# Performance work log

Hardware: AMD Instinct MI355X
Metric: run time of the kernel (lower is better)

The kernel has to match this reference:

```python
import jax, jax.numpy as jnp
import numpy as np

EMB = 1024
HEADS = 16
HEAD_DIM = EMB // HEADS
DIM_FF = 4096
EPS = 1e-05


def layer_norm(x, gain, bias):
    # BasicLayerNorm: (x - mean) / (std + eps), std with unbiased=False
    mean = jnp.mean(x, axis=-1, keepdims=True)
    std = jnp.sqrt(jnp.mean((x - mean) ** 2, axis=-1, keepdims=True))
    return gain * ((x - mean) / (std + EPS)) + bias


def setup_inputs() -> dict:
    key = jax.random.key(0)
    ks = jax.random.split(key, 8)
    scale = 1.0 / np.sqrt(EMB)
    x = jax.random.normal(ks[0], (4, 2048, EMB), dtype=jnp.float32)
    Wq = jax.random.normal(ks[1], (EMB, EMB), dtype=jnp.float32) * scale
    Wk = jax.random.normal(ks[2], (EMB, EMB), dtype=jnp.float32) * scale
    Wv = jax.random.normal(ks[3], (EMB, EMB), dtype=jnp.float32) * scale
    Wo = jax.random.normal(ks[4], (EMB, EMB), dtype=jnp.float32) * scale
    W1 = jax.random.normal(ks[5], (EMB, DIM_FF), dtype=jnp.float32) * scale
    b1 = jnp.zeros((DIM_FF,), dtype=jnp.float32)
    W2 = jax.random.normal(ks[6], (DIM_FF, EMB), dtype=jnp.float32) * (1.0 / np.sqrt(DIM_FF))
    b2 = jnp.zeros((EMB,), dtype=jnp.float32)
    gain1 = jnp.ones((EMB,), dtype=jnp.float32)
    bias1 = jnp.zeros((EMB,), dtype=jnp.float32)
    gain2 = jnp.ones((EMB,), dtype=jnp.float32)
    bias2 = jnp.zeros((EMB,), dtype=jnp.float32)
    return dict(x=x, Wq=Wq, Wk=Wk, Wv=Wv, Wo=Wo, W1=W1, b1=b1, W2=W2, b2=b2,
                gain1=gain1, bias1=bias1, gain2=gain2, bias2=bias2)


def reference(x, Wq, Wk, Wv, Wo, W1, b1, W2, b2, gain1, bias1, gain2, bias2):
    b, t, e = x.shape
    h, dk = HEADS, HEAD_DIM
    # QKV projections, split heads -> (b, h, t, dk)
    q = (x @ Wq).reshape(b, t, h, dk).transpose(0, 2, 1, 3)
    k = (x @ Wk).reshape(b, t, h, dk).transpose(0, 2, 1, 3)
    v = (x @ Wv).reshape(b, t, h, dk).transpose(0, 2, 1, 3)
    # scaled dot-product attention
    scores = jnp.einsum('bhqd,bhkd->bhqk', q, k) / jnp.sqrt(jnp.float32(dk))
    attn = jax.nn.softmax(scores, axis=-1)
    ctx = jnp.einsum('bhqk,bhkd->bhqd', attn, v)
    # merge heads and output projection
    merged = ctx.transpose(0, 2, 1, 3).reshape(b, t, e)
    attended = merged @ Wo
    # residual + layer norm 1 (dropout is identity at inference)
    x1 = layer_norm(attended + x, gain1, bias1)
    # feed-forward
    ff = jax.nn.relu(x1 @ W1 + b1) @ W2 + b2
    # residual + layer norm 2
    return layer_norm(ff + x1, gain2, bias2)
```

## Files before the change

kernel.cpp:

```cpp
#include <hip/hip_runtime.h>
#include <hip/hip_bf16.h>
#include <math.h>

#define EMB 1024
#define DIM_FF 4096
#define HEADS 16
#define HD 64
#define TSEQ 2048
#define BATCH 4
#define MROWS (BATCH*TSEQ)
#define LN_EPS 1e-5f

typedef __attribute__((ext_vector_type(8))) short short8;
typedef __attribute__((ext_vector_type(4))) float f32x4;

#define MFMA16(a,b,c) __builtin_amdgcn_mfma_f32_16x16x32_bf16((a),(b),(c),0,0,0)

#define GLOBAL_AS(p) ((const __attribute__((address_space(1))) void*)(p))
#define LDS_AS(p)    ((__attribute__((address_space(3))) void*)(p))

__device__ __forceinline__ unsigned short bf16bits(float f){
    __hip_bfloat16 h = __float2bfloat16(f);
    unsigned short u;
    __builtin_memcpy(&u, &h, 2);
    return u;
}
__device__ __forceinline__ unsigned cvtpk_bf16(float lo, float hi){
    unsigned r;
    asm("v_cvt_pk_bf16_f32 %0, %1, %2" : "=v"(r) : "v"(lo), "v"(hi));
    return r;
}
__device__ __forceinline__ f32x4 ld4bf(const __hip_bfloat16* p){
    ushort4 u = *reinterpret_cast<const ushort4*>(p);
    union{unsigned i; float f;} c0,c1,c2,c3;
    c0.i=(unsigned)u.x<<16; c1.i=(unsigned)u.y<<16; c2.i=(unsigned)u.z<<16; c3.i=(unsigned)u.w<<16;
    f32x4 r; r[0]=c0.f; r[1]=c1.f; r[2]=c2.f; r[3]=c3.f;
    return r;
}

__global__ __launch_bounds__(256)
void cvt_bf16(const float* __restrict__ in, __hip_bfloat16* __restrict__ out, int n4){
    int i = blockIdx.x*256 + threadIdx.x;
    if (i >= n4) return;
    f32x4 v = reinterpret_cast<const f32x4*>(in)[i];
    uint2 o;
    o.x = cvtpk_bf16(v[0], v[1]);
    o.y = cvtpk_bf16(v[2], v[3]);
    *reinterpret_cast<uint2*>(reinterpret_cast<unsigned short*>(out) + (size_t)i*4) = o;
}

__global__ __launch_bounds__(256)
void transpose_cvt4(const float* __restrict__ s0, const float* __restrict__ s1,
                    const float* __restrict__ s2, const float* __restrict__ s3,
                    __hip_bfloat16* __restrict__ out){
    const float* in = blockIdx.z==0 ? s0 : blockIdx.z==1 ? s1 : blockIdx.z==2 ? s2 : s3;
    __hip_bfloat16* dst = out + (size_t)blockIdx.z*1024*1024;
    __shared__ __hip_bfloat16 tile[32][33];
    int bx = blockIdx.x*32, by = blockIdx.y*32;
    int x = bx + threadIdx.x;
    #pragma unroll
    for (int i = threadIdx.y; i < 32; i += 8)
        tile[i][threadIdx.x] = __float2bfloat16(in[(size_t)(by+i)*1024 + x]);
    __syncthreads();
    int xo = by + threadIdx.x;
    #pragma unroll
    for (int i = threadIdx.y; i < 32; i += 8)
        dst[(size_t)(bx+i)*1024 + xo] = tile[threadIdx.x][i];
}

__global__ __launch_bounds__(256)
void transpose_cvt(const float* __restrict__ in, __hip_bfloat16* __restrict__ out, int R, int C){
    __shared__ __hip_bfloat16 tile[32][33];
    int bx = blockIdx.x*32, by = blockIdx.y*32;
    int x = bx + threadIdx.x;
    #pragma unroll
    for (int i = threadIdx.y; i < 32; i += 8)
        tile[i][threadIdx.x] = __float2bfloat16(in[(size_t)(by+i)*C + x]);
    __syncthreads();
    int xo = by + threadIdx.x;
    #pragma unroll
    for (int i = threadIdx.y; i < 32; i += 8)
        out[(size_t)(bx+i)*R + xo] = tile[threadIdx.x][i];
}

template<int EPI>
__global__ __launch_bounds__(256, 2)
void gemm_bt(const __hip_bfloat16* __restrict__ A,
             const __hip_bfloat16* __restrict__ Bt,
             int M, int N, int K,
             __hip_bfloat16* __restrict__ Cb,
             const float* __restrict__ bias)
{
    __shared__ __align__(16) __hip_bfloat16 As[128*32];
    __shared__ __align__(16) __hip_bfloat16 Bs[128*32];
    const int tid = threadIdx.x;
    const int lane = tid & 63;
    const int wid = tid >> 6;
    const int wm = wid >> 1, wn = wid & 1;
    const int row0 = blockIdx.x * 128;
    const int col0 = blockIdx.y * 128;
    const int rA = lane & 15, kg = lane >> 4;

    const int lrow = lane >> 2;
    const int lcol = (lane & 3) << 3;

    f32x4 acc[4][4] = {};

    for (int kt = 0; kt < K; kt += 32) {
        __syncthreads();
        #pragma unroll
        for (int half = 0; half < 2; ++half) {
            const int rbase = (wid << 5) + (half << 4);
            const int r = rbase + lrow;
            __builtin_amdgcn_global_load_lds(
                GLOBAL_AS(A + (size_t)(row0 + r)*K + kt + lcol),
                LDS_AS(&As[rbase*32]), 16, 0, 0);
            __builtin_amdgcn_global_load_lds(
                GLOBAL_AS(Bt + (size_t)(col0 + r)*K + kt + lcol),
                LDS_AS(&Bs[rbase*32]), 16, 0, 0);
        }
        __syncthreads();
        short8 af[4], bfr[4];
        #pragma unroll
        for (int mi = 0; mi < 4; ++mi)
            af[mi] = *reinterpret_cast<const short8*>(&As[(wm*64 + mi*16 + rA)*32 + (kg<<3)]);
        #pragma unroll
        for (int ni = 0; ni < 4; ++ni)
            bfr[ni] = *reinterpret_cast<const short8*>(&Bs[(wn*64 + ni*16 + rA)*32 + (kg<<3)]);
        #pragma unroll
        for (int mi = 0; mi < 4; ++mi)
            #pragma unroll
            for (int ni = 0; ni < 4; ++ni)
                acc[mi][ni] = MFMA16(af[mi], bfr[ni], acc[mi][ni]);
    }

    #pragma unroll
    for (int mi=0; mi<4; ++mi) {
        #pragma unroll
        for (int ni=0; ni<4; ++ni) {
            #pragma unroll
            for (int j=0;j<4;++j){
                float v = acc[mi][ni][j];
                int grow = row0 + wm*64 + mi*16 + (kg<<2) + j;
                int gcol = col0 + wn*64 + ni*16 + rA;
                if constexpr (EPI==3) v += bias[gcol];
                Cb[(size_t)grow*N + gcol] = __float2bfloat16(v);
            }
        }
    }
}

#define GPHASE(P, STAGE_EXPR, WAIT_EXPR) do { \
    short8 af[2][2]; \
    _Pragma("unroll") \
    for (int i_=0;i_<2;++i_){ \
      _Pragma("unroll") \
      for (int kk_=0;kk_<2;++kk_) \
        af[i_][kk_] = *reinterpret_cast<const short8*>(pA + ((2*(P)+i_)*16+rA)*128 + (((kk_<<2)+kg)^swz)*16); \
    } \
    STAGE_EXPR; WAIT_EXPR; \
    __builtin_amdgcn_s_barrier(); \
    __builtin_amdgcn_s_setprio(1); \
    _Pragma("unroll") \
    for (int i_=0;i_<2;++i_){ \
      _Pragma("unroll") \
      for (int ni_=0;ni_<4;++ni_){ \
        acc[2*(P)+i_][ni_] = MFMA16(af[i_][0], bfr[ni_][0], acc[2*(P)+i_][ni_]); \
        acc[2*(P)+i_][ni_] = MFMA16(af[i_][1], bfr[ni_][1], acc[2*(P)+i_][ni_]); \
      } \
    } \
    __builtin_amdgcn_s_setprio(0); \
    __builtin_amdgcn_s_barrier(); \
} while(0)

template<int EPI>
__global__ __launch_bounds__(512, 2)
void gemm256(const __hip_bfloat16* __restrict__ A,
             const __hip_bfloat16* __restrict__ Bt,
             int M, int N, int K,
             __hip_bfloat16* __restrict__ Cb,
             const float* __restrict__ bias,
             __hip_bfloat16* __restrict__ qo,
             __hip_bfloat16* __restrict__ ko,
             __hip_bfloat16* __restrict__ vto)
{
    __shared__ __align__(16) __hip_bfloat16 Al[2][16384];
    __shared__ __align__(16) __hip_bfloat16 Bl[2][16384];
    const int tid = threadIdx.x;
    const int lane = tid & 63;
    const int wid = tid >> 6;
    const int wm = wid >> 2, wn = wid & 3;
    const int row0 = blockIdx.x * 256;
    const int col0 = blockIdx.y * 256;
    const int rA = lane & 15, kg = lane >> 4, swz = rA & 7;
    const int NT = K >> 6;

    const int lr = lane >> 3;
    const int lg = (lane & 7) ^ lr;
    const __hip_bfloat16* sA = A  + (size_t)(row0 + wid*8 + lr)*K + lg*8;
    const __hip_bfloat16* sB = Bt + (size_t)(col0 + wid*8 + lr)*K + lg*8;
    char* dA = (char*)&Al[0][0] + wid*8*128;
    char* dB = (char*)&Bl[0][0] + wid*8*128;

    auto stage = [&](const __hip_bfloat16* s, char* d, int buf, int half, int kt){
        #pragma unroll
        for (int rr = 0; rr < 2; ++rr)
            __builtin_amdgcn_global_load_lds(
                GLOBAL_AS(s + (size_t)(half*128 + rr*64)*K + kt),
                LDS_AS(d + buf*32768 + (half*128 + rr*64)*128), 16, 0, 0);
    };

    f32x4 acc[8][4] = {};

    stage(sA, dA, 0, 0, 0); stage(sA, dA, 0, 1, 0);
    stage(sB, dB, 0, 0, 0); stage(sB, dB, 0, 1, 0);
    stage(sB, dB, 1, 0, 64); stage(sB, dB, 1, 1, 64);
    asm volatile("s_waitcnt vmcnt(4)" ::: "memory");
    __builtin_amdgcn_sched_barrier(0);
    __builtin_amdgcn_s_barrier();

    const char* cA = (const char*)&Al[0][0] + wm*128*128;
    const char* cB = (const char*)&Bl[0][0] + wn*64*128;

    for (int t = 0; t < NT; ++t) {
        const int buf = t & 1;
        const char* pA = cA + buf*32768;
        const char* pB = cB + buf*32768;
        short8 bfr[4][2];
        #pragma unroll
        for (int ni = 0; ni < 4; ++ni)
            #pragma unroll
            for (int kk = 0; kk < 2; ++kk)
                bfr[ni][kk] = *reinterpret_cast<const short8*>(pB + (ni*16+rA)*128 + (((kk<<2)+kg)^swz)*16);

        GPHASE(0, if (t+1 < NT) stage(sA, dA, buf^1, 0, (t+1)*64), );
        GPHASE(1, if (t+1 < NT) stage(sA, dA, buf^1, 1, (t+1)*64), );
        GPHASE(2, if (t+2 < NT) stage(sB, dB, buf,   0, (t+2)*64), );
        GPHASE(3, if (t+2 < NT) stage(sB, dB, buf,   1, (t+2)*64),
            if (t+2 < NT) { asm volatile("s_waitcnt vmcnt(4)" ::: "memory"); }
            else          { asm volatile("s_waitcnt vmcnt(0)" ::: "memory"); }
            __builtin_amdgcn_sched_barrier(0) );
    }

    #pragma unroll
    for (int mi=0; mi<8; ++mi) {
        #pragma unroll
        for (int ni=0; ni<4; ++ni) {
            #pragma unroll
            for (int j=0;j<4;++j){
                float v = acc[mi][ni][j];
                int grow = row0 + wm*128 + mi*16 + (kg<<2) + j;
                int gcol = col0 + wn*64 + ni*16 + rA;
                if constexpr (EPI==0) {
                    int b = grow >> 11, t = grow & 2047;
                    int which = gcol >> 10, hdx = gcol & 1023;
                    int h = hdx >> 6, d = hdx & 63;
                    int bh = b*HEADS + h;
                    if (which==0)      qo[((size_t)bh*TSEQ + t)*HD + d] = __float2bfloat16(v*0.125f);
                    else if (which==1) ko[((size_t)bh*TSEQ + t)*HD + d] = __float2bfloat16(v);
                    else               vto[((size_t)bh*HD + d)*TSEQ + t] = __float2bfloat16(v);
                } else {
                    v += bias[gcol]; v = v > 0.0f ? v : 0.0f;
                    Cb[(size_t)grow*N + gcol] = __float2bfloat16(v);
                }
            }
        }
    }
}

__global__ __launch_bounds__(256, 4)
void attn_fwd(const __hip_bfloat16* __restrict__ q,
              const __hip_bfloat16* __restrict__ k,
              const __hip_bfloat16* __restrict__ vt,
              __hip_bfloat16* __restrict__ merged)
{
    const int wg = (blockIdx.x & 7) * 256 + (blockIdx.x >> 3);
    const int bh = wg >> 5;
    const int qt = wg & 31;
    const int wid = threadIdx.x >> 6, lane = threadIdx.x & 63;
    const int rA = lane & 15, kg = lane >> 4;
    const int qrow0 = qt*64 + wid*16;
    const __hip_bfloat16* Qh = q  + (size_t)bh*TSEQ*HD;
    const __hip_bfloat16* Kh = k  + (size_t)bh*TSEQ*HD;
    const __hip_bfloat16* Vh = vt + (size_t)bh*HD*TSEQ;

    __shared__ __align__(16) __hip_bfloat16 Kl[2][64*64];
    __shared__ __align__(16) __hip_bfloat16 Vl[2][64*64];
    __shared__ __align__(16) __hip_bfloat16 plds[4][8][16][8];

    short8 aQ0 = *reinterpret_cast<const short8*>(Qh + (size_t)(qrow0+rA)*HD + (kg<<3));
    short8 aQ1 = *reinterpret_cast<const short8*>(Qh + (size_t)(qrow0+rA)*HD + 32 + (kg<<3));

    const int lrow = lane >> 3;
    const int lslot = ((lane & 7) ^ lrow) << 3;
    const __hip_bfloat16* sK0 = Kh + (size_t)(wid*16 + lrow)*HD + lslot;
    const __hip_bfloat16* sV0 = Vh + (size_t)(wid*16 + lrow)*TSEQ + lslot;
    const int dOff = wid*16*64;

    f32x4 O[4] = {};
    float m = -1e30f, lpart = 0.f;
    const int swz = rA & 7;

    {
        __builtin_amdgcn_global_load_lds(GLOBAL_AS(sK0),          LDS_AS(&Kl[0][dOff]),        16, 0, 0);
        __builtin_amdgcn_global_load_lds(GLOBAL_AS(sK0 + 8*HD),   LDS_AS(&Kl[0][dOff + 8*64]), 16, 0, 0);
        __builtin_amdgcn_global_load_lds(GLOBAL_AS(sV0),          LDS_AS(&Vl[0][dOff]),        16, 0, 0);
        __builtin_amdgcn_global_load_lds(GLOBAL_AS(sV0 + 8*TSEQ), LDS_AS(&Vl[0][dOff + 8*64]), 16, 0, 0);
    }
    __syncthreads();

    for (int t = 0; t < TSEQ/64; ++t) {
        const int b = t & 1;
        if (t < TSEQ/64 - 1) {
            const int kt = (t+1)*64;
            __builtin_amdgcn_global_load_lds(GLOBAL_AS(sK0 + (size_t)kt*HD),     LDS_AS(&Kl[b^1][dOff]),        16, 0, 0);
            __builtin_amdgcn_global_load_lds(GLOBAL_AS(sK0 + (size_t)(kt+8)*HD), LDS_AS(&Kl[b^1][dOff + 8*64]), 16, 0, 0);
            __builtin_amdgcn_global_load_lds(GLOBAL_AS(sV0 + kt),                LDS_AS(&Vl[b^1][dOff]),        16, 0, 0);
            __builtin_amdgcn_global_load_lds(GLOBAL_AS(sV0 + 8*TSEQ + kt),       LDS_AS(&Vl[b^1][dOff + 8*64]), 16, 0, 0);
        }
        const char* Kb = (const char*)&Kl[b][0];
        const char* Vb = (const char*)&Vl[b][0];

        f32x4 st[4];
        #pragma unroll
        for (int kb = 0; kb < 4; ++kb) {
            const int ro = (kb*16 + rA) * 128;
            short8 aK0 = *reinterpret_cast<const short8*>(Kb + ro + ((kg ^ swz) << 4));
            short8 aK1 = *reinterpret_cast<const short8*>(Kb + ro + (((4+kg) ^ swz) << 4));
            f32x4 z = {};
            z = MFMA16(aK0, aQ0, z);
            st[kb] = MFMA16(aK1, aQ1, z);
        }
        f32x4 m4 = st[0];
        #pragma unroll
        for (int kb=1; kb<4; ++kb)
            #pragma unroll
            for (int j=0;j<4;++j) m4[j] = fmaxf(m4[j], st[kb][j]);
        float mx = fmaxf(fmaxf(m4[0], m4[1]), fmaxf(m4[2], m4[3]));
        mx = fmaxf(mx, __shfl_xor(mx, 16));
        mx = fmaxf(mx, __shfl_xor(mx, 32));
        if (!__all(mx - m <= 8.0f)) {
            float mn = fmaxf(m, mx);
            float al = __expf(m - mn);
            lpart *= al;
            float alq[4];
            #pragma unroll
            for (int j=0;j<4;++j) alq[j] = __shfl(al, (kg<<2)+j);
            #pragma unroll
            for (int dt=0; dt<4; ++dt)
                #pragma unroll
                for (int j=0;j<4;++j) O[dt][j] *= alq[j];
            m = mn;
        }
        f32x4 ps[4];
        #pragma unroll
        for (int kb=0; kb<4; ++kb)
            #pragma unroll
            for (int j=0;j<4;++j)
                ps[kb][j] = __expf(st[kb][j] - m);
        f32x4 ssv = (ps[0]+ps[1]) + (ps[2]+ps[3]);
        lpart += (ssv[0]+ssv[1]) + (ssv[2]+ssv[3]);
        #pragma unroll
        for (int kb=0; kb<4; ++kb) {
            uint2 w;
            w.x = cvtpk_bf16(ps[kb][0], ps[kb][1]);
            w.y = cvtpk_bf16(ps[kb][2], ps[kb][3]);
            *reinterpret_cast<uint2*>(&plds[wid][2*kb + (kg>>1)][rA][(kg&1)<<2]) = w;
        }
        short8 aP0 = *reinterpret_cast<const short8*>(&plds[wid][kg][rA][0]);
        short8 aP1 = *reinterpret_cast<const short8*>(&plds[wid][4+kg][rA][0]);
        #pragma unroll
        for (int dt=0; dt<4; ++dt) {
            const int vo = (dt*16 + rA) * 128;
            short8 bV0 = *reinterpret_cast<const short8*>(Vb + vo + ((kg ^ swz) << 4));
            short8 bV1 = *reinterpret_cast<const short8*>(Vb + vo + (((4+kg) ^ swz) << 4));
            O[dt] = MFMA16(aP0, bV0, O[dt]);
            O[dt] = MFMA16(aP1, bV1, O[dt]);
        }
        __syncthreads();
    }

    float lrow_ = lpart;
    lrow_ += __shfl_xor(lrow_, 16);
    lrow_ += __shfl_xor(lrow_, 32);
    float lq[4];
    #pragma unroll
    for (int j=0;j<4;++j) lq[j] = 1.0f / __shfl(lrow_, (kg<<2)+j);
    const int b = bh >> 4, h = bh & 15;
    #pragma unroll
    for (int dt=0; dt<4; ++dt){
        #pragma unroll
        for (int j=0;j<4;++j){
            int t = qrow0 + (kg<<2) + j;
            int col = h*HD + dt*16 + rA;
            merged[((size_t)(b*TSEQ + t))*EMB + col] = __float2bfloat16(O[dt][j]*lq[j]);
        }
    }
}

template<int ABF, int RBF>
__global__ __launch_bounds__(256)
void ln_res(const void* __restrict__ a_, const void* __restrict__ res_,
            const float* __restrict__ gain, const float* __restrict__ bias,
            float* __restrict__ outf, __hip_bfloat16* __restrict__ outb)
{
    const int row = blockIdx.x;
    const int tid = threadIdx.x;
    const int lane = tid & 63, wid = tid >> 6;
    const size_t base = (size_t)row * EMB;
    f32x4 va, vr;
    if constexpr (ABF) va = ld4bf((const __hip_bfloat16*)a_ + base + tid*4);
    else               va = *reinterpret_cast<const f32x4*>((const float*)a_ + base + tid*4);
    if constexpr (RBF) vr = ld4bf((const __hip_bfloat16*)res_ + base + tid*4);
    else               vr = *reinterpret_cast<const f32x4*>((const float*)res_ + base + tid*4);
    f32x4 v = va + vr;
    float s = v[0]+v[1]+v[2]+v[3];
    #pragma unroll
    for (int off=1; off<64; off<<=1) s += __shfl_xor(s, off);
    __shared__ float red1[4], red2[4];
    if (lane==0) red1[wid] = s;
    __syncthreads();
    float mean = (red1[0]+red1[1]+red1[2]+red1[3]) * (1.0f/EMB);
    f32x4 d;
    #pragma unroll
    for (int j=0;j<4;++j) d[j] = v[j] - mean;
    float qs = d[0]*d[0]+d[1]*d[1]+d[2]*d[2]+d[3]*d[3];
    #pragma unroll
    for (int off=1; off<64; off<<=1) qs += __shfl_xor(qs, off);
    if (lane==0) red2[wid] = qs;
    __syncthreads();
    float var = (red2[0]+red2[1]+red2[2]+red2[3]) * (1.0f/EMB);
    float r = 1.0f/(sqrtf(var)+LN_EPS);
    f32x4 g = *reinterpret_cast<const f32x4*>(gain + tid*4);
    f32x4 bb = *reinterpret_cast<const f32x4*>(bias + tid*4);
    f32x4 o;
    #pragma unroll
    for (int j=0;j<4;++j) o[j] = g[j]*(d[j]*r) + bb[j];
    if (outf)
        *reinterpret_cast<f32x4*>(outf + base + tid*4) = o;
    if (outb) {
        uint2 ob;
        ob.x = cvtpk_bf16(o[0], o[1]);
        ob.y = cvtpk_bf16(o[2], o[3]);
        *reinterpret_cast<uint2*>(reinterpret_cast<unsigned short*>(outb) + base + tid*4) = ob;
    }
}

extern "C" void kernel_launch(void* const* d_in, const int* in_sizes, int n_in,
                              void* d_out, int out_size, void* d_ws, size_t ws_size,
                              hipStream_t stream) {
    const float* x   = (const float*)d_in[0];
    const float* Wq  = (const float*)d_in[1];
    const float* Wk  = (const float*)d_in[2];
    const float* Wv  = (const float*)d_in[3];
    const float* Wo  = (const float*)d_in[4];
    const float* W1  = (const float*)d_in[5];
    const float* b1  = (const float*)d_in[6];
    const float* W2  = (const float*)d_in[7];
    const float* b2  = (const float*)d_in[8];
    const float* gain1 = (const float*)d_in[9];
    const float* bias1 = (const float*)d_in[10];
    const float* gain2 = (const float*)d_in[11];
    const float* bias2 = (const float*)d_in[12];

    char* ws = (char*)d_ws;
    __hip_bfloat16* Wqkv_t   = (__hip_bfloat16*)(ws + 0);
    __hip_bfloat16* Wo_t     = (__hip_bfloat16*)(ws + 6291456);
    __hip_bfloat16* W1_t     = (__hip_bfloat16*)(ws + 8388608);
    __hip_bfloat16* W2_t     = (__hip_bfloat16*)(ws + 16777216);
    __hip_bfloat16* xb       = (__hip_bfloat16*)(ws + 25165824);
    __hip_bfloat16* qb       = (__hip_bfloat16*)(ws + 41943040);
    __hip_bfloat16* kbuf     = (__hip_bfloat16*)(ws + 58720256);
    __hip_bfloat16* vtb      = (__hip_bfloat16*)(ws + 75497472);
    __hip_bfloat16* h1       = (__hip_bfloat16*)(ws + 25165824);
    __hip_bfloat16* mergedb  = (__hip_bfloat16*)(ws + 92274688);
    __hip_bfloat16* ffb      = (__hip_bfloat16*)(ws + 92274688);
    __hip_bfloat16* attendedb= (__hip_bfloat16*)(ws + 109051904);
    __hip_bfloat16* x1b      = (__hip_bfloat16*)(ws + 125829120);
    float*          outf     = (float*)d_out;

    dim3 tb(32,8);
    transpose_cvt4<<<dim3(32,32,4), tb, 0, stream>>>(Wq, Wk, Wv, Wo, Wqkv_t);
    transpose_cvt<<<dim3(128,32), tb, 0, stream>>>(W1, W1_t, 1024, 4096);
    transpose_cvt<<<dim3(32,128), tb, 0, stream>>>(W2, W2_t, 4096, 1024);
    cvt_bf16<<<(MROWS*EMB/4 + 255)/256, 256, 0, stream>>>(x, xb, MROWS*EMB/4);

    gemm256<0><<<dim3(MROWS/256, 3072/256), 512, 0, stream>>>(
        xb, Wqkv_t, MROWS, 3072, EMB, nullptr, nullptr, qb, kbuf, vtb);
    attn_fwd<<<dim3(2048), 256, 0, stream>>>(qb, kbuf, vtb, mergedb);
    gemm_bt<1><<<dim3(MROWS/128, EMB/128), 256, 0, stream>>>(
        mergedb, Wo_t, MROWS, EMB, EMB, attendedb, nullptr);
    ln_res<1,0><<<MROWS, 256, 0, stream>>>(attendedb, x, gain1, bias1, nullptr, x1b);
    gemm256<2><<<dim3(MROWS/256, DIM_FF/256), 512, 0, stream>>>(
        x1b, W1_t, MROWS, DIM_FF, EMB, h1, b1, nullptr, nullptr, nullptr);
    gemm_bt<3><<<dim3(MROWS/128, EMB/128), 256, 0, stream>>>(
        h1, W2_t, MROWS, EMB, DIM_FF, ffb, b2);
    ln_res<1,1><<<MROWS, 256, 0, stream>>>(ffb, x1b, gain2, bias2, outf, nullptr);
}
```

Before: 442.6 us.

## Rewrite attention with 32x32 MFMA tiles, register P exchange, and exp2 softmax

The attention kernel now uses 32x32x16 bf16 MFMA, so each wave handles 32 query rows and each block handles 128, and the grid is halved. The P matrix moves between the two MFMA layouts through cross-lane shuffles instead of an LDS round trip. Q is pre-scaled by log2(e)/8 so softmax can use exp2 directly. The aim is to get more reuse of each K/V tile loaded into LDS, fewer LDS operations and cheaper exponentials, at the cost of more registers and fewer blocks in flight.

```diff
diff --git a/kernel.cpp b/kernel.cpp
--- a/kernel.cpp
+++ b/kernel.cpp
@@ -10,21 +10,18 @@
 #define BATCH 4
 #define MROWS (BATCH*TSEQ)
 #define LN_EPS 1e-5f
+#define QSCALE 0.18033688011f
 
 typedef __attribute__((ext_vector_type(8))) short short8;
 typedef __attribute__((ext_vector_type(4))) float f32x4;
+typedef __attribute__((ext_vector_type(16))) float f32x16;
 
 #define MFMA16(a,b,c) __builtin_amdgcn_mfma_f32_16x16x32_bf16((a),(b),(c),0,0,0)
+#define MFMA32(a,b,c) __builtin_amdgcn_mfma_f32_32x32x16_bf16((a),(b),(c),0,0,0)
 
 #define GLOBAL_AS(p) ((const __attribute__((address_space(1))) void*)(p))
 #define LDS_AS(p)    ((__attribute__((address_space(3))) void*)(p))
 
-__device__ __forceinline__ unsigned short bf16bits(float f){
-    __hip_bfloat16 h = __float2bfloat16(f);
-    unsigned short u;
-    __builtin_memcpy(&u, &h, 2);
-    return u;
-}
 __device__ __forceinline__ unsigned cvtpk_bf16(float lo, float hi){
     unsigned r;
     asm("v_cvt_pk_bf16_f32 %0, %1, %2" : "=v"(r) : "v"(lo), "v"(hi));
@@ -256,7 +253,7 @@
                     int which = gcol >> 10, hdx = gcol & 1023;
                     int h = hdx >> 6, d = hdx & 63;
                     int bh = b*HEADS + h;
-                    if (which==0)      qo[((size_t)bh*TSEQ + t)*HD + d] = __float2bfloat16(v*0.125f);
+                    if (which==0)      qo[((size_t)bh*TSEQ + t)*HD + d] = __float2bfloat16(v*QSCALE);
                     else if (which==1) ko[((size_t)bh*TSEQ + t)*HD + d] = __float2bfloat16(v);
                     else               vto[((size_t)bh*HD + d)*TSEQ + t] = __float2bfloat16(v);
                 } else {
@@ -274,22 +271,25 @@
               const __hip_bfloat16* __restrict__ vt,
               __hip_bfloat16* __restrict__ merged)
 {
-    const int wg = (blockIdx.x & 7) * 256 + (blockIdx.x >> 3);
-    const int bh = wg >> 5;
-    const int qt = wg & 31;
+    const int wg = (blockIdx.x & 7) * 128 + (blockIdx.x >> 3);
+    const int bh = wg >> 4;
+    const int qt = wg & 15;
     const int wid = threadIdx.x >> 6, lane = threadIdx.x & 63;
-    const int rA = lane & 15, kg = lane >> 4;
-    const int qrow0 = qt*64 + wid*16;
+    const int l31 = lane & 31;
+    const int hi  = lane >> 5;
+    const int swz = lane & 7;
+    const int qrow0 = qt*128 + wid*32;
     const __hip_bfloat16* Qh = q  + (size_t)bh*TSEQ*HD;
     const __hip_bfloat16* Kh = k  + (size_t)bh*TSEQ*HD;
     const __hip_bfloat16* Vh = vt + (size_t)bh*HD*TSEQ;
 
     __shared__ __align__(16) __hip_bfloat16 Kl[2][64*64];
     __shared__ __align__(16) __hip_bfloat16 Vl[2][64*64];
-    __shared__ __align__(16) __hip_bfloat16 plds[4][8][16][8];
-
-    short8 aQ0 = *reinterpret_cast<const short8*>(Qh + (size_t)(qrow0+rA)*HD + (kg<<3));
-    short8 aQ1 = *reinterpret_cast<const short8*>(Qh + (size_t)(qrow0+rA)*HD + 32 + (kg<<3));
+
+    short8 qv[4];
+    #pragma unroll
+    for (int c=0;c<4;++c)
+        qv[c] = *reinterpret_cast<const short8*>(Qh + (size_t)(qrow0+l31)*HD + c*16 + hi*8);
 
     const int lrow = lane >> 3;
     const int lslot = ((lane & 7) ^ lrow) << 3;
@@ -297,9 +297,8 @@
     const __hip_bfloat16* sV0 = Vh + (size_t)(wid*16 + lrow)*TSEQ + lslot;
     const int dOff = wid*16*64;
 
-    f32x4 O[4] = {};
+    f32x16 O0 = {}, O1 = {};
     float m = -1e30f, lpart = 0.f;
-    const int swz = rA & 7;
 
     {
         __builtin_amdgcn_global_load_lds(GLOBAL_AS(sK0),          LDS_AS(&Kl[0][dOff]),        16, 0, 0);
@@ -321,80 +320,84 @@
         const char* Kb = (const char*)&Kl[b][0];
         const char* Vb = (const char*)&Vl[b][0];
 
-        f32x4 st[4];
-        #pragma unroll
-        for (int kb = 0; kb < 4; ++kb) {
-            const int ro = (kb*16 + rA) * 128;
-            short8 aK0 = *reinterpret_cast<const short8*>(Kb + ro + ((kg ^ swz) << 4));
-            short8 aK1 = *reinterpret_cast<const short8*>(Kb + ro + (((4+kg) ^ swz) << 4));
-            f32x4 z = {};
-            z = MFMA16(aK0, aQ0, z);
-            st[kb] = MFMA16(aK1, aQ1, z);
-        }
-        f32x4 m4 = st[0];
-        #pragma unroll
-        for (int kb=1; kb<4; ++kb)
+        f32x16 st0 = {}, st1 = {};
+        #pragma unroll
+        for (int c=0;c<4;++c) {
+            short8 ka0 = *reinterpret_cast<const short8*>(Kb + l31*128        + (((2*c+hi)^swz)<<4));
+            short8 ka1 = *reinterpret_cast<const short8*>(Kb + (32+l31)*128   + (((2*c+hi)^swz)<<4));
+            st0 = MFMA32(ka0, qv[c], st0);
+            st1 = MFMA32(ka1, qv[c], st1);
+        }
+
+        float mr[16];
+        #pragma unroll
+        for (int r=0;r<16;++r) mr[r] = fmaxf(st0[r], st1[r]);
+        #pragma unroll
+        for (int s=8; s>0; s>>=1)
             #pragma unroll
-            for (int j=0;j<4;++j) m4[j] = fmaxf(m4[j], st[kb][j]);
-        float mx = fmaxf(fmaxf(m4[0], m4[1]), fmaxf(m4[2], m4[3]));
-        mx = fmaxf(mx, __shfl_xor(mx, 16));
+            for (int i=0;i<8;++i) if (i<s) mr[i] = fmaxf(mr[i], mr[i+s]);
+        float mx = mr[0];
         mx = fmaxf(mx, __shfl_xor(mx, 32));
+
         if (!__all(mx - m <= 8.0f)) {
             float mn = fmaxf(m, mx);
-            float al = __expf(m - mn);
+            float al = __builtin_amdgcn_exp2f(m - mn);
             lpart *= al;
-            float alq[4];
             #pragma unroll
-            for (int j=0;j<4;++j) alq[j] = __shfl(al, (kg<<2)+j);
-            #pragma unroll
-            for (int dt=0; dt<4; ++dt)
-                #pragma unroll
-                for (int j=0;j<4;++j) O[dt][j] *= alq[j];
+            for (int r=0;r<16;++r) {
+                float alr = __shfl(al, (r&3) + 8*(r>>2) + 4*hi);
+                O0[r] *= alr; O1[r] *= alr;
+            }
             m = mn;
         }
-        f32x4 ps[4];
-        #pragma unroll
-        for (int kb=0; kb<4; ++kb)
-            #pragma unroll
-            for (int j=0;j<4;++j)
-                ps[kb][j] = __expf(st[kb][j] - m);
-        f32x4 ssv = (ps[0]+ps[1]) + (ps[2]+ps[3]);
-        lpart += (ssv[0]+ssv[1]) + (ssv[2]+ssv[3]);
-        #pragma unroll
-        for (int kb=0; kb<4; ++kb) {
-            uint2 w;
-            w.x = cvtpk_bf16(ps[kb][0], ps[kb][1]);
-            w.y = cvtpk_bf16(ps[kb][2], ps[kb][3]);
-            *reinterpret_cast<uint2*>(&plds[wid][2*kb + (kg>>1)][rA][(kg&1)<<2]) = w;
-        }
-        short8 aP0 = *reinterpret_cast<const short8*>(&plds[wid][kg][rA][0]);
-        short8 aP1 = *reinterpret_cast<const short8*>(&plds[wid][4+kg][rA][0]);
-        #pragma unroll
-        for (int dt=0; dt<4; ++dt) {
-            const int vo = (dt*16 + rA) * 128;
-            short8 bV0 = *reinterpret_cast<const short8*>(Vb + vo + ((kg ^ swz) << 4));
-            short8 bV1 = *reinterpret_cast<const short8*>(Vb + vo + (((4+kg) ^ swz) << 4));
-            O[dt] = MFMA16(aP0, bV0, O[dt]);
-            O[dt] = MFMA16(aP1, bV1, O[dt]);
+        #pragma unroll
+        for (int r=0;r<16;++r) {
+            st0[r] = __builtin_amdgcn_exp2f(st0[r] - m);
+            st1[r] = __builtin_amdgcn_exp2f(st1[r] - m);
+        }
+        {
+            f32x16 ss = st0 + st1;
+            float s8 = (((ss[0]+ss[1])+(ss[2]+ss[3]))+((ss[4]+ss[5])+(ss[6]+ss[7])))
+                     + (((ss[8]+ss[9])+(ss[10]+ss[11]))+((ss[12]+ss[13])+(ss[14]+ss[15])));
+            lpart += s8;
+        }
+        unsigned pk0[8], pk1[8];
+        #pragma unroll
+        for (int j=0;j<8;++j) {
+            pk0[j] = cvtpk_bf16(st0[2*j], st0[2*j+1]);
+            pk1[j] = cvtpk_bf16(st1[2*j], st1[2*j+1]);
+        }
+        #pragma unroll
+        for (int kc=0; kc<4; ++kc) {
+            const unsigned* pkt = (kc>>1) ? pk1 : pk0;
+            const int j0 = 4*(kc&1);
+            unsigned swA = (unsigned)__shfl_xor((int)pkt[j0+0], 32);
+            unsigned swB = (unsigned)__shfl_xor((int)pkt[j0+1], 32);
+            unsigned swC = (unsigned)__shfl_xor((int)pkt[j0+2], 32);
+            unsigned swD = (unsigned)__shfl_xor((int)pkt[j0+3], 32);
+            union { unsigned u[4]; short8 s; } pa;
+            pa.u[0] = hi ? swC : pkt[j0+0];
+            pa.u[1] = hi ? swD : pkt[j0+1];
+            pa.u[2] = hi ? pkt[j0+2] : swA;
+            pa.u[3] = hi ? pkt[j0+3] : swB;
+            short8 vf0 = *reinterpret_cast<const short8*>(Vb + l31*128      + (((2*kc+hi)^swz)<<4));
+            short8 vf1 = *reinterpret_cast<const short8*>(Vb + (32+l31)*128 + (((2*kc+hi)^swz)<<4));
+            O0 = MFMA32(pa.s, vf0, O0);
+            O1 = MFMA32(pa.s, vf1, O1);
         }
         __syncthreads();
     }
 
-    float lrow_ = lpart;
-    lrow_ += __shfl_xor(lrow_, 16);
-    lrow_ += __shfl_xor(lrow_, 32);
-    float lq[4];
-    #pragma unroll
-    for (int j=0;j<4;++j) lq[j] = 1.0f / __shfl(lrow_, (kg<<2)+j);
+    lpart += __shfl_xor(lpart, 32);
+    float linv = 1.0f / lpart;
     const int b = bh >> 4, h = bh & 15;
     #pragma unroll
-    for (int dt=0; dt<4; ++dt){
-        #pragma unroll
-        for (int j=0;j<4;++j){
-            int t = qrow0 + (kg<<2) + j;
-            int col = h*HD + dt*16 + rA;
-            merged[((size_t)(b*TSEQ + t))*EMB + col] = __float2bfloat16(O[dt][j]*lq[j]);
-        }
+    for (int r=0;r<16;++r){
+        int qp = (r&3) + 8*(r>>2) + 4*hi;
+        float lr = __shfl(linv, qp);
+        size_t base = ((size_t)(b*TSEQ + qrow0 + qp))*EMB + h*HD;
+        merged[base + l31]      = __float2bfloat16(O0[r]*lr);
+        merged[base + 32 + l31] = __float2bfloat16(O1[r]*lr);
     }
 }
 
@@ -487,7 +490,7 @@
 
     gemm256<0><<<dim3(MROWS/256, 3072/256), 512, 0, stream>>>(
         xb, Wqkv_t, MROWS, 3072, EMB, nullptr, nullptr, qb, kbuf, vtb);
-    attn_fwd<<<dim3(2048), 256, 0, stream>>>(qb, kbuf, vtb, mergedb);
+    attn_fwd<<<dim3(1024), 256, 0, stream>>>(qb, kbuf, vtb, mergedb);
     gemm_bt<1><<<dim3(MROWS/128, EMB/128), 256, 0, stream>>>(
         mergedb, Wo_t, MROWS, EMB, EMB, attendedb, nullptr);
     ln_res<1,0><<<MROWS, 256, 0, stream>>>(attendedb, x, gain1, bias1, nullptr, x1b);
```

After: 426.2 us. -3.7%, faster.
